# Performance work log

Hardware: AMD Instinct MI355X
Metric: run time of the kernel (lower is better)

The kernel has to match this reference:

```python
import jax, jax.numpy as jnp
import numpy as np

H, C = 4, 32          # GAT heads, per-head dim
NH = 4                # transformer heads


def layer_norm(x, g, b, eps=1e-5):
    mu = x.mean(-1, keepdims=True)
    var = ((x - mu) ** 2).mean(-1, keepdims=True)
    return (x - mu) / jnp.sqrt(var + eps) * g + b


def setup_inputs() -> dict:
    key = jax.random.key(0)
    ks = jax.random.split(key, 16)
    B, T, N, F = 256, 72, 5, 10
    D, FF = 128, 256
    # full directed graph on 5 stations, no self loops (E=20)
    ei = np.array([[i, j] for i in range(N) for j in range(N) if i != j], dtype=np.int32).T
    s = 0.1
    return {
        'x': jax.random.normal(ks[0], (B, T, N, F), jnp.float32),
        'edge_index': jnp.asarray(ei),
        'gcn_w': jax.random.normal(ks[1], (F, 64), jnp.float32) * s,
        'gcn_b': jnp.zeros((64,), jnp.float32),
        'gat_w': jax.random.normal(ks[2], (64, H * C), jnp.float32) * s,
        'gat_a_src': jax.random.normal(ks[3], (H, C), jnp.float32) * s,
        'gat_a_dst': jax.random.normal(ks[4], (H, C), jnp.float32) * s,
        'gat_b': jnp.zeros((H * C,), jnp.float32),
        'gln_g': jnp.ones((D,), jnp.float32),
        'gln_b': jnp.zeros((D,), jnp.float32),
        'tw_qkv': jax.random.normal(ks[5], (3, D, 3 * D), jnp.float32) * s,
        'tb_qkv': jnp.zeros((3, 3 * D), jnp.float32),
        'tw_o': jax.random.normal(ks[6], (3, D, D), jnp.float32) * s,
        'tb_o': jnp.zeros((3, D), jnp.float32),
        'ln1_g': jnp.ones((3, D), jnp.float32),
        'ln1_b': jnp.zeros((3, D), jnp.float32),
        'w_ff1': jax.random.normal(ks[7], (3, D, FF), jnp.float32) * s,
        'b_ff1': jnp.zeros((3, FF), jnp.float32),
        'w_ff2': jax.random.normal(ks[8], (3, FF, D), jnp.float32) * s,
        'b_ff2': jnp.zeros((3, D), jnp.float32),
        'ln2_g': jnp.ones((3, D), jnp.float32),
        'ln2_b': jnp.zeros((3, D), jnp.float32),
        'hw1': jax.random.normal(ks[9], (6, D, D // 2), jnp.float32) * s,
        'hb1': jnp.zeros((6, D // 2), jnp.float32),
        'hw2': jax.random.normal(ks[10], (6, D // 2, 5), jnp.float32) * s,
        'hb2': jnp.zeros((6, 5), jnp.float32),
    }


def reference(x, edge_index, gcn_w, gcn_b, gat_w, gat_a_src, gat_a_dst, gat_b,
              gln_g, gln_b, tw_qkv, tb_qkv, tw_o, tb_o, ln1_g, ln1_b,
              w_ff1, b_ff1, w_ff2, b_ff2, ln2_g, ln2_b, hw1, hb1, hw2, hb2):
    B, T, N, F = x.shape
    D = gln_g.shape[0]

    # ---- frozen GCN encoder (torch.no_grad): symmetric-normalized A with self loops
    src, dst = edge_index[0], edge_index[1]
    loop = jnp.arange(N, dtype=src.dtype)
    src2 = jnp.concatenate([src, loop])
    dst2 = jnp.concatenate([dst, loop])
    A = jnp.zeros((N, N), x.dtype).at[dst2, src2].add(1.0)
    deg = A.sum(1)
    dinv = jnp.where(deg > 0, deg ** -0.5, 0.0)
    Anorm = dinv[:, None] * A * dinv[None, :]
    xw = jnp.einsum('btnf,fh->btnh', x, gcn_w) + gcn_b
    gcn = jnp.tanh(jnp.einsum('ij,btjh->btih', Anorm, xw))
    gcn = jax.lax.stop_gradient(gcn)  # encoder is frozen + no_grad

    # ---- GATConv over batched graph (self loops added, PyG default), eval mode (no dropout)
    h = jnp.einsum('btnf,fhc->btnhc', gcn, gat_w.reshape(gcn.shape[-1], H, C))
    a_s = (h * gat_a_src).sum(-1)                         # [B,T,N,H]
    a_d = (h * gat_a_dst).sum(-1)
    e = a_s[:, :, src2, :] + a_d[:, :, dst2, :]           # [B,T,E2,H]
    e = jnp.where(e > 0, e, 0.2 * e)                      # LeakyReLU(0.2)
    eT = jnp.moveaxis(e, 2, 0)                            # [E2,B,T,H]
    m = jax.ops.segment_max(eT, dst2, num_segments=N)
    ex = jnp.exp(eT - m[dst2])
    denom = jax.ops.segment_sum(ex, dst2, num_segments=N)
    alpha = ex / denom[dst2]                              # scatter-softmax per dst node
    hsrc = jnp.moveaxis(h, 2, 0)[src2]                    # [E2,B,T,H,C]
    agg = jax.ops.segment_sum(alpha[..., None] * hsrc, dst2, num_segments=N)
    gat = jnp.moveaxis(agg, 0, 2).reshape(B, T, N, H * C) + gat_b
    gat = layer_norm(gat, gln_g, gln_b)

    # ---- mean-pool stations, positional encoding
    z = gat.mean(2)                                       # [B,T,D]
    pos = jnp.arange(T, dtype=jnp.float32)[:, None]
    div = jnp.exp(jnp.arange(0, D, 2, dtype=jnp.float32) * (-np.log(10000.0) / D))
    pe = jnp.zeros((T, D), x.dtype).at[:, 0::2].set(jnp.sin(pos * div)).at[:, 1::2].set(jnp.cos(pos * div))
    z = z + pe

    # ---- post-norm transformer encoder (relu FF), eval mode
    dh = D // NH
    scale = jnp.sqrt(jnp.asarray(dh, x.dtype))
    for i in range(tw_qkv.shape[0]):
        qkv = z @ tw_qkv[i] + tb_qkv[i]
        q, k, v = jnp.split(qkv, 3, axis=-1)
        q = q.reshape(B, T, NH, dh)
        k = k.reshape(B, T, NH, dh)
        v = v.reshape(B, T, NH, dh)
        att = jax.nn.softmax(jnp.einsum('bqhd,bkhd->bhqk', q, k) / scale, axis=-1)
        o = jnp.einsum('bhqk,bkhd->bqhd', att, v).reshape(B, T, D)
        z = layer_norm(z + o @ tw_o[i] + tb_o[i], ln1_g[i], ln1_b[i])
        ff = jax.nn.relu(z @ w_ff1[i] + b_ff1[i]) @ w_ff2[i] + b_ff2[i]
        z = layer_norm(z + ff, ln2_g[i], ln2_b[i])

    # ---- multi-horizon forecast heads on last timestep -> stacked [6,B,5]
    last = z[:, -1]
    h1 = jax.nn.relu(jnp.einsum('bd,kdm->kbm', last, hw1) + hb1[:, None, :])
    out = jnp.einsum('kbm,kms->kbs', h1, hw2) + hb2[:, None, :]
    return out
```

## Files before the change

### kernel.cpp

```cpp
#include <hip/hip_runtime.h>
#include <hip/hip_bf16.h>

#define B_  256
#define T_  72
#define N_  5
#define F_  10
#define D_  128
#define HH_ 4
#define CC_ 32
#define FF_ 256
#define BT_ (B_*T_)
#define E2MAX 32

#define WS_Z    256
#define WS_QKV  (WS_Z + BT_*D_)
#define WS_OBUF (WS_QKV + BT_*3*D_)
#define WS_WBF  (WS_OBUF + BT_*D_)

#define WOFF_QKV(i)  ((i)*49152)
#define WOFF_O(i)    (147456 + (i)*16384)
#define WOFF_FF1(i)  (196608 + (i)*32768)
#define WOFF_FF2(i)  (294912 + (i)*32768)
#define WOFF_GATW    393216

typedef __attribute__((ext_vector_type(8))) short bf16x8;
typedef __attribute__((ext_vector_type(4))) float f32x4;

__device__ __forceinline__ unsigned short bf16_rne(float x) {
    unsigned u = __float_as_uint(x);
    unsigned r = (u + 0x7FFFu + ((u >> 16) & 1u)) >> 16;
    return (unsigned short)r;
}
__device__ __forceinline__ unsigned bf16pk(float a, float b) {
    return (unsigned)bf16_rne(a) | ((unsigned)bf16_rne(b) << 16);
}
__device__ __forceinline__ float bf2f(short s) {
    return __uint_as_float(((unsigned)(unsigned short)s) << 16);
}

__global__ void setup_kernel(const int* __restrict__ ei, float* __restrict__ ws, int E) {
    if (threadIdx.x != 0 || blockIdx.x != 0) return;
    int* wsi = (int*)ws;
    const int N = N_;
    int E2 = E + N;
    int src2[E2MAX], dst2[E2MAX];
    for (int e = 0; e < E; ++e) { src2[e] = ei[e]; dst2[e] = ei[E + e]; }
    for (int n = 0; n < N; ++n) { src2[E + n] = n; dst2[E + n] = n; }
    float A[N_ * N_];
    for (int i = 0; i < N * N; ++i) A[i] = 0.f;
    for (int e = 0; e < E2; ++e) A[dst2[e] * N + src2[e]] += 1.f;
    float dinv[N_];
    for (int n = 0; n < N; ++n) {
        float s = 0.f;
        for (int j = 0; j < N; ++j) s += A[n * N + j];
        dinv[n] = (s > 0.f) ? rsqrtf(s) : 0.f;
    }
    for (int n = 0; n < N; ++n)
        for (int j = 0; j < N; ++j)
            ws[n * N + j] = dinv[n] * A[n * N + j] * dinv[j];
    int cnt[N_];
    for (int n = 0; n < N; ++n) cnt[n] = 0;
    for (int e = 0; e < E2; ++e) cnt[dst2[e]]++;
    int off = 0;
    for (int n = 0; n < N; ++n) { wsi[96 + n] = off; off += cnt[n]; }
    wsi[96 + N] = off;
    int cur[N_];
    for (int n = 0; n < N; ++n) cur[n] = wsi[96 + n];
    for (int e = 0; e < E2; ++e) wsi[104 + cur[dst2[e]]++] = e;
    for (int e = 0; e < E2; ++e) { wsi[32 + e] = src2[e]; wsi[64 + e] = dst2[e]; }
}
// ... 3 lines not shown
    const float* __restrict__ w_ff1, const float* __restrict__ w_ff2,
    const float* __restrict__ gat_w, short* __restrict__ wbf)
{
    __shared__ float s_t[64][65];
    const int tid = threadIdx.x;
    int t = blockIdx.x;
    const float* src; short* dst; int R, C, tr, tc;
    if (t >= 96) { int q = t - 96; src = gat_w; dst = wbf + WOFF_GATW; R = 64; C = 128; tr = 0; tc = q; }
    else {
        int layer = t / 32, r32 = t % 32;
        if (r32 < 12)      { src = tw_qkv + layer * (128*384); dst = wbf + WOFF_QKV(layer); R = 128; C = 384; tr = r32 / 6;  tc = r32 % 6; }
        else if (r32 < 16) { int q = r32 - 12; src = tw_o + layer * 16384; dst = wbf + WOFF_O(layer);  R = 128; C = 128; tr = q >> 1; tc = q & 1; }
        else if (r32 < 24) { int q = r32 - 16; src = w_ff1 + layer * 32768; dst = wbf + WOFF_FF1(layer); R = 128; C = 256; tr = q >> 2; tc = q & 3; }
        else               { int q = r32 - 24; src = w_ff2 + layer * 32768; dst = wbf + WOFF_FF2(layer); R = 256; C = 128; tr = q >> 1; tc = q & 1; }
    }
    #pragma unroll
    for (int it = 0; it < 16; ++it) {
        int e = it * 256 + tid;
        int r = e >> 6, c = e & 63;
        s_t[r][c] = src[(size_t)(tr*64 + r) * C + tc*64 + c];
    }
    __syncthreads();
    #pragma unroll
    for (int it = 0; it < 16; ++it) {
        int e = it * 256 + tid;
        int c = e >> 6, r = e & 63;
        dst[(size_t)(tc*64 + c) * R + tr*64 + r] = (short)bf16_rne(s_t[r][c]);
    }
}

__device__ __forceinline__ bf16x8 ld_frag(const short* s, int row, int kbase, int ldk) {
    return *(const bf16x8*)&s[row * ldk + (kbase ^ ((row & 7) << 3))];
}
__device__ __forceinline__ void stage_a(short* s_a, const float* __restrict__ src, int tid) {
    const float2* s2 = (const float2*)src;
    #pragma unroll
    for (int it = 0; it < 16; ++it) {
        int i2 = it * 256 + tid;
        int row = i2 >> 6, ke = (i2 & 63) * 2;
        float2 v = s2[i2];
        *(unsigned*)&s_a[row * 128 + (ke ^ ((row & 7) << 3))] = bf16pk(v.x, v.y);
    }
}
__device__ __forceinline__ void stage_b(short* s_b, const short* __restrict__ src, int tid) {
    const uint4* s4 = (const uint4*)src;
    #pragma unroll
    for (int it = 0; it < 8; ++it) {
        int c = it * 256 + tid;
        int row = c >> 4, ke = (c & 15) * 8;
        *(uint4*)&s_b[row * 128 + (ke ^ ((row & 7) << 3))] = s4[c];
    }
}

__global__ __launch_bounds__(256) void gcn_h_mfma(
    const float* __restrict__ x, const float* __restrict__ gcn_w, const float* __restrict__ gcn_b,
    const float* __restrict__ a_src, const float* __restrict__ a_dst,
    const float* __restrict__ ws, const short* __restrict__ gwT,
    short* __restrict__ hbuf, float* __restrict__ asb, float* __restrict__ adb)
{
    __shared__ float s_x[16 * 50];
    __shared__ float s_an[25];
    __shared__ short s_gcn[80 * 64];

    const int tid = threadIdx.x;
    const int tok0 = blockIdx.x * 16;

    for (int i = tid; i < 16 * 50; i += 256) s_x[i] = x[(size_t)tok0 * 50 + i];
    if (tid < 25) s_an[tid] = ws[tid];
    __syncthreads();

    #pragma unroll
    for (int it = 0; it < 2; ++it) {
        int idx = it * 256 + tid;
        int tl = idx >> 5, kp = idx & 31;
        int k0 = kp * 2;
        float w0[F_], w1[F_];
// ... 137 lines not shown
            a0 += s_alpha[wv][e][h0] * bf2f(s_h[rb + lane]);
            a1 += s_alpha[wv][e][h1] * bf2f(s_h[rb + lane + 64]);
        }
        v0[n] = a0 + gb0; v1[n] = a1 + gb1;
    }
    float r1[N_], r2[N_];
    #pragma unroll
    for (int n = 0; n < N_; ++n) { r1[n] = v0[n] + v1[n]; r2[n] = v0[n]*v0[n] + v1[n]*v1[n]; }
    #pragma unroll
    for (int mm = 1; mm < 64; mm <<= 1)
        #pragma unroll
        for (int n = 0; n < N_; ++n) { r1[n] += __shfl_xor(r1[n], mm); r2[n] += __shfl_xor(r2[n], mm); }
    float z0 = 0.f, z1 = 0.f;
    #pragma unroll
    for (int n = 0; n < N_; ++n) {
        float mu = r1[n] * (1.f / D_);
        float var = r2[n] * (1.f / D_) - mu * mu;
        float rstd = rsqrtf(var + 1e-5f);
        z0 += (v0[n] - mu) * rstd * gg0 + gB0;
        z1 += (v1[n] - mu) * rstd * gg1 + gB1;
    }
    z0 *= (1.f / N_); z1 *= (1.f / N_);
    const float cpe = -9.210340371976184f / (float)D_;
    int t = tok % T_;
    float dv0 = __expf((float)(lane & ~1) * cpe);
    float dv1 = __expf((float)((lane + 64) & ~1) * cpe);
    float ang0 = (float)t * dv0, ang1 = (float)t * dv1;
    z0 += (lane & 1) ? __cosf(ang0) : __sinf(ang0);
    z1 += (lane & 1) ? __cosf(ang1) : __sinf(ang1);
    z[(size_t)tok * D_ + lane] = z0;
    z[(size_t)tok * D_ + 64 + lane] = z1;
}

__global__ __launch_bounds__(256) void qkv_mfma(
    const float* __restrict__ z, const short* __restrict__ WT, const float* __restrict__ bias,
    float* __restrict__ qkv)
{
    __shared__ short s_a[64 * 128];
    __shared__ short s_b[128 * 128];
    const int tid = threadIdx.x;
    const int w = tid >> 6, lane = tid & 63;
    const int tok0 = blockIdx.x * 64;
    stage_a(s_a, z + (size_t)tok0 * 128, tid);
    __syncthreads();
    bf16x8 af[4];
    const int arow = w * 16 + (lane & 15);
    const int kf = (lane >> 4) * 8;
    #pragma unroll
    for (int k0 = 0; k0 < 4; ++k0) af[k0] = ld_frag(s_a, arow, k0 * 32 + kf, 128);

    for (int ch = 0; ch < 3; ++ch) {
        __syncthreads();
        stage_b(s_b, WT + ch * 128 * 128, tid);
        __syncthreads();
        #pragma unroll
        for (int n0 = 0; n0 < 8; ++n0) {
            const int ncol = ch * 128 + n0 * 16 + (lane & 15);
            const int brow = n0 * 16 + (lane & 15);
            float bv = bias[ncol];
            f32x4 acc = {bv, bv, bv, bv};
            #pragma unroll
            for (int k0 = 0; k0 < 4; ++k0) {
                bf16x8 bfg = ld_frag(s_b, brow, k0 * 32 + kf, 128);
                acc = __builtin_amdgcn_mfma_f32_16x16x32_bf16(af[k0], bfg, acc, 0, 0, 0);
            }
            const int r0 = tok0 + w * 16 + (lane >> 4) * 4;
            #pragma unroll
            for (int i = 0; i < 4; ++i)
                qkv[(size_t)(r0 + i) * 384 + ncol] = acc[i];
        }
    }
}

__global__ __launch_bounds__(256) void attn_mfma(
    const float* __restrict__ qkv, float* __restrict__ obuf)
{
    __shared__ short s_q[80 * 40];
    __shared__ short s_k[80 * 40];
    __shared__ short s_vt[32 * 104];
    __shared__ short s_p[80 * 104];

    const int bh = blockIdx.x;
    const int b = bh >> 2, h = bh & 3;
    const int tid = threadIdx.x;
    const int w = tid >> 6, lane = tid & 63;
    const int c = lane & 15, g = lane >> 4;
    const float* base = qkv + (size_t)b * T_ * 384 + h * 32;

    for (int idx = tid; idx < 80 * 32; idx += 256) {
        int row = idx >> 5, cc = idx & 31;
        float qv = 0.f, kv = 0.f;
        if (row < T_) {
            qv = base[row * 384 + cc];
            kv = base[row * 384 + 128 + cc];
        }
        s_q[row * 40 + cc] = (short)bf16_rne(qv);
        s_k[row * 40 + cc] = (short)bf16_rne(kv);
    }
    for (int idx = tid; idx < 80 * 32; idx += 256) {
        int key = idx >> 5, cc = idx & 31;
        float vv = (key < T_) ? base[key * 384 + 256 + cc] : 0.f;
        s_vt[cc * 104 + key] = (short)bf16_rne(vv);
    }
    for (int idx = tid; idx < 32 * 24; idx += 256) {
        int cc = idx / 24, key = 80 + idx % 24;
        s_vt[cc * 104 + key] = 0;
    }
    for (int idx = tid; idx < 80 * 24; idx += 256) {
        int row = idx / 24, col = 80 + idx % 24;
        s_p[row * 104 + col] = 0;
    }
    __syncthreads();

    const float scale = 0.17677669529663687f;

    for (int m = w; m < 5; m += 4) {
        bf16x8 aq = *(const bf16x8*)&s_q[(m * 16 + c) * 40 + g * 8];
        f32x4 accS[5];
        #pragma unroll
        for (int n0 = 0; n0 < 5; ++n0) {
            bf16x8 bk = *(const bf16x8*)&s_k[(n0 * 16 + c) * 40 + g * 8];
            f32x4 z4 = {0,0,0,0};
            accS[n0] = __builtin_amdgcn_mfma_f32_16x16x32_bf16(aq, bk, z4, 0, 0, 0);
        }
        float ps[5][4];
        float mx[4], den[4];
        #pragma unroll
        for (int i = 0; i < 4; ++i) mx[i] = -1e30f;
        #pragma unroll
        for (int n0 = 0; n0 < 5; ++n0)
            #pragma unroll
            for (int i = 0; i < 4; ++i) {
                float s = accS[n0][i] * scale;
                if (n0 == 4 && c >= 8) s = -1e30f;
                ps[n0][i] = s;
                mx[i] = fmaxf(mx[i], s);
            }
        #pragma unroll
        for (int mm = 1; mm < 16; mm <<= 1)
            #pragma unroll
            for (int i = 0; i < 4; ++i) mx[i] = fmaxf(mx[i], __shfl_xor(mx[i], mm));
        #pragma unroll
        for (int i = 0; i < 4; ++i) den[i] = 0.f;
        #pragma unroll
        for (int n0 = 0; n0 < 5; ++n0)
            #pragma unroll
            for (int i = 0; i < 4; ++i) {
                float e = __expf(ps[n0][i] - mx[i]);
                ps[n0][i] = e;
                den[i] += e;
            }
        #pragma unroll
        for (int mm = 1; mm < 16; mm <<= 1)
            #pragma unroll
            for (int i = 0; i < 4; ++i) den[i] += __shfl_xor(den[i], mm);
        float rden[4];
        #pragma unroll
        for (int i = 0; i < 4; ++i) rden[i] = 1.f / den[i];
        #pragma unroll
        for (int n0 = 0; n0 < 5; ++n0)
            #pragma unroll
            for (int i = 0; i < 4; ++i) {
                int row = m * 16 + g * 4 + i;
                s_p[row * 104 + n0 * 16 + c] = (short)bf16_rne(ps[n0][i] * rden[i]);
            }
        f32x4 accO[2] = {{0,0,0,0},{0,0,0,0}};
        #pragma unroll
        for (int kt = 0; kt < 3; ++kt) {
            bf16x8 ap = *(const bf16x8*)&s_p[(m * 16 + c) * 104 + kt * 32 + g * 8];
            #pragma unroll
            for (int n0 = 0; n0 < 2; ++n0) {
                bf16x8 bv = *(const bf16x8*)&s_vt[(n0 * 16 + c) * 104 + kt * 32 + g * 8];
                accO[n0] = __builtin_amdgcn_mfma_f32_16x16x32_bf16(ap, bv, accO[n0], 0, 0, 0);
            }
        }
        #pragma unroll
        for (int n0 = 0; n0 < 2; ++n0)
            #pragma unroll
            for (int i = 0; i < 4; ++i) {
                int row = m * 16 + g * 4 + i;
                if (row < T_)
                    obuf[(size_t)(b * T_ + row) * D_ + h * 32 + n0 * 16 + c] = accO[n0][i];
            }
    }
}

__global__ __launch_bounds__(256) void oproj_ff_mfma(
    const float* __restrict__ obuf, const short* __restrict__ WoT, const float* __restrict__ bo,
    const float* __restrict__ g1, const float* __restrict__ be1,
    const short* __restrict__ W1T, const float* __restrict__ b1,
    const short* __restrict__ W2T, const float* __restrict__ b2,
    const float* __restrict__ g2, const float* __restrict__ be2,
    float* __restrict__ z)
{
    __shared__ short s_a[64 * 128];
    __shared__ short s_b[128 * 128];
    __shared__ short s_f[64 * 256];
    const int tid = threadIdx.x;
    const int w = tid >> 6, lane = tid & 63;
    const int tok0 = blockIdx.x * 64;
    const int cbase = lane & 15;
    const int arow = w * 16 + cbase;
    const int kf = (lane >> 4) * 8;
    const int r0 = tok0 + w * 16 + (lane >> 4) * 4;
    const int lrow0 = w * 16 + (lane >> 4) * 4;

    stage_a(s_a, obuf + (size_t)tok0 * 128, tid);
    stage_b(s_b, WoT, tid);
    __syncthreads();
    bf16x8 af[4];
    #pragma unroll
    for (int k0 = 0; k0 < 4; ++k0) af[k0] = ld_frag(s_a, arow, k0 * 32 + kf, 128);

    f32x4 acc[8];
    #pragma unroll
    for (int n0 = 0; n0 < 8; ++n0) {
        float bv = bo[n0 * 16 + cbase];
        acc[n0] = (f32x4){bv, bv, bv, bv};
        const int brow = n0 * 16 + cbase;
        #pragma unroll
        for (int k0 = 0; k0 < 4; ++k0) {
            bf16x8 bfg = ld_frag(s_b, brow, k0 * 32 + kf, 128);
            acc[n0] = __builtin_amdgcn_mfma_f32_16x16x32_bf16(af[k0], bfg, acc[n0], 0, 0, 0);
        }
    }
    #pragma unroll
    for (int n0 = 0; n0 < 8; ++n0)
        #pragma unroll
        for (int i = 0; i < 4; ++i)
            acc[n0][i] += z[(size_t)(r0 + i) * 128 + n0 * 16 + cbase];
    {
        float s1[4] = {0,0,0,0}, s2[4] = {0,0,0,0};
        #pragma unroll
        for (int n0 = 0; n0 < 8; ++n0)
            #pragma unroll
            for (int i = 0; i < 4; ++i) { float v = acc[n0][i]; s1[i] += v; s2[i] += v * v; }
        #pragma unroll
        for (int m = 1; m < 16; m <<= 1)
            #pragma unroll
            for (int i = 0; i < 4; ++i) { s1[i] += __shfl_xor(s1[i], m); s2[i] += __shfl_xor(s2[i], m); }
        #pragma unroll
        for (int i = 0; i < 4; ++i) {
            float mu = s1[i] * (1.f / D_);
            float var = s2[i] * (1.f / D_) - mu * mu;
            float rstd = rsqrtf(var + 1e-5f);
            #pragma unroll
            for (int n0 = 0; n0 < 8; ++n0) {
                float gv = g1[n0 * 16 + cbase], bev = be1[n0 * 16 + cbase];
                acc[n0][i] = (acc[n0][i] - mu) * rstd * gv + bev;
            }
        }
    }
    #pragma unroll
    for (int n0 = 0; n0 < 8; ++n0)
        #pragma unroll
        for (int i = 0; i < 4; ++i) {
            int row = lrow0 + i;
            s_a[row * 128 + ((n0 * 16 + cbase) ^ ((row & 7) << 3))] = (short)bf16_rne(acc[n0][i]);
        }
    bf16x8 af1[4];
    #pragma unroll
    for (int k0 = 0; k0 < 4; ++k0) af1[k0] = ld_frag(s_a, arow, k0 * 32 + kf, 128);

    for (int ch = 0; ch < 2; ++ch) {
        __syncthreads();
        stage_b(s_b, W1T + ch * 128 * 128, tid);
        __syncthreads();
        #pragma unroll
        for (int n0 = 0; n0 < 8; ++n0) {
            const int ncol = ch * 128 + n0 * 16 + cbase;
            const int brow = n0 * 16 + cbase;
            float bv = b1[ncol];
            f32x4 a = {bv, bv, bv, bv};
            #pragma unroll
            for (int k0 = 0; k0 < 4; ++k0) {
                bf16x8 bfg = ld_frag(s_b, brow, k0 * 32 + kf, 128);
                a = __builtin_amdgcn_mfma_f32_16x16x32_bf16(af1[k0], bfg, a, 0, 0, 0);
            }
            #pragma unroll
            for (int i = 0; i < 4; ++i) {
                int row = lrow0 + i;
                s_f[row * 256 + (ncol ^ ((row & 7) << 3))] = (short)bf16_rne(fmaxf(a[i], 0.f));
            }
        }
    }
    f32x4 acc2[8];
    #pragma unroll
    for (int n0 = 0; n0 < 8; ++n0) {
        float bv = b2[n0 * 16 + cbase];
        acc2[n0] = (f32x4){bv, bv, bv, bv};
    }
    for (int kc = 0; kc < 2; ++kc) {
        __syncthreads();
        #pragma unroll
        for (int it = 0; it < 8; ++it) {
            int cc = it * 256 + tid;
            int row = cc >> 4, ke = (cc & 15) * 8;
            uint4 v = *(const uint4*)&W2T[row * 256 + kc * 128 + ke];
            *(uint4*)&s_b[row * 128 + (ke ^ ((row & 7) << 3))] = v;
        }
        __syncthreads();
        bf16x8 af2[4];
        #pragma unroll
        for (int k0 = 0; k0 < 4; ++k0)
            af2[k0] = ld_frag(s_f, arow, kc * 128 + k0 * 32 + kf, 256);
        #pragma unroll
        for (int n0 = 0; n0 < 8; ++n0) {
            const int brow = n0 * 16 + cbase;
            #pragma unroll
            for (int k0 = 0; k0 < 4; ++k0) {
                bf16x8 bfg = ld_frag(s_b, brow, k0 * 32 + kf, 128);
                acc2[n0] = __builtin_amdgcn_mfma_f32_16x16x32_bf16(af2[k0], bfg, acc2[n0], 0, 0, 0);
            }
        }
    }
    #pragma unroll
    for (int n0 = 0; n0 < 8; ++n0)
        #pragma unroll
        for (int i = 0; i < 4; ++i)
            acc2[n0][i] += acc[n0][i];
    float s1[4] = {0,0,0,0}, s2[4] = {0,0,0,0};
    #pragma unroll
    for (int n0 = 0; n0 < 8; ++n0)
        #pragma unroll
        for (int i = 0; i < 4; ++i) { float v = acc2[n0][i]; s1[i] += v; s2[i] += v * v; }
    #pragma unroll
    for (int m = 1; m < 16; m <<= 1)
        #pragma unroll
        for (int i = 0; i < 4; ++i) { s1[i] += __shfl_xor(s1[i], m); s2[i] += __shfl_xor(s2[i], m); }
    #pragma unroll
    for (int i = 0; i < 4; ++i) {
        float mu = s1[i] * (1.f / D_);
        float var = s2[i] * (1.f / D_) - mu * mu;
        float rstd = rsqrtf(var + 1e-5f);
        #pragma unroll
        for (int n0 = 0; n0 < 8; ++n0) {
            float gv = g2[n0 * 16 + cbase], bev = be2[n0 * 16 + cbase];
            z[(size_t)(r0 + i) * 128 + n0 * 16 + cbase] = (acc2[n0][i] - mu) * rstd * gv + bev;
        }
    }
}

__global__ __launch_bounds__(64) void heads_kernel(
    const float* __restrict__ z, const float* __restrict__ hw1, const float* __restrict__ hb1,
    const float* __restrict__ hw2, const float* __restrict__ hb2, float* __restrict__ out)
{
    const int k = blockIdx.x >> 8;
    const int b = blockIdx.x & 255;
    const int tid = threadIdx.x;
    __shared__ float s_last[D_];
    __shared__ float s_h1[64];
    const float* zr = z + (size_t)(b * T_ + (T_ - 1)) * D_;
    s_last[tid] = zr[tid];
    s_last[tid + 64] = zr[tid + 64];
    __syncthreads();
    float acc = hb1[k * 64 + tid];
    const float* w1 = hw1 + (size_t)k * D_ * 64;
    for (int dd = 0; dd < D_; ++dd) acc += s_last[dd] * w1[dd * 64 + tid];
    s_h1[tid] = fmaxf(acc, 0.f);
    __syncthreads();
    if (tid < 5) {
        float o = hb2[k * 5 + tid];
        const float* w2 = hw2 + (size_t)k * 64 * 5;
        for (int j = 0; j < 64; ++j) o += s_h1[j] * w2[j * 5 + tid];
        out[(size_t)k * (B_ * 5) + b * 5 + tid] = o;
    }
}

extern "C" void kernel_launch(void* const* d_in, const int* in_sizes, int n_in,
                              void* d_out, int out_size, void* d_ws, size_t ws_size,
                              hipStream_t stream) {
    const float* x      = (const float*)d_in[0];
    const int*   ei     = (const int*)  d_in[1];
    const float* gcn_w  = (const float*)d_in[2];
    const float* gcn_b  = (const float*)d_in[3];
    const float* gat_w  = (const float*)d_in[4];
    const float* a_src  = (const float*)d_in[5];
    const float* a_dst  = (const float*)d_in[6];
    const float* gat_b  = (const float*)d_in[7];
    const float* gln_g  = (const float*)d_in[8];
    const float* gln_b  = (const float*)d_in[9];
    const float* tw_qkv = (const float*)d_in[10];
    const float* tb_qkv = (const float*)d_in[11];
    const float* tw_o   = (const float*)d_in[12];
    const float* tb_o   = (const float*)d_in[13];
    const float* ln1_g  = (const float*)d_in[14];
    const float* ln1_b  = (const float*)d_in[15];
    const float* w_ff1  = (const float*)d_in[16];
    const float* b_ff1  = (const float*)d_in[17];
    const float* w_ff2  = (const float*)d_in[18];
    const float* b_ff2  = (const float*)d_in[19];
    const float* ln2_g  = (const float*)d_in[20];
    const float* ln2_b  = (const float*)d_in[21];
    const float* hw1    = (const float*)d_in[22];
    const float* hb1    = (const float*)d_in[23];
    const float* hw2    = (const float*)d_in[24];
    const float* hb2    = (const float*)d_in[25];
    float* out = (float*)d_out;
    float* ws  = (float*)d_ws;

    float* z    = ws + WS_Z;
    float* qkv  = ws + WS_QKV;
    float* obuf = ws + WS_OBUF;
    short* wbf  = (short*)(ws + WS_WBF);

    short* hbuf = (short*)(ws + WS_QKV);
    float* asb  = ws + WS_OBUF;
    float* adb  = ws + WS_OBUF + BT_ * 5 * 4;

    const int E = in_sizes[1] / 2;
    const int E2 = E + N_;

    setup_kernel<<<1, 64, 0, stream>>>(ei, ws, E);
    prep_kernel<<<98, 256, 0, stream>>>(tw_qkv, tw_o, w_ff1, w_ff2, gat_w, wbf);
    gcn_h_mfma<<<BT_ / 16, 256, 0, stream>>>(x, gcn_w, gcn_b, a_src, a_dst, ws,
                                             wbf + WOFF_GATW, hbuf, asb, adb);
    gat_agg<<<BT_ / 4, 256, 0, stream>>>(hbuf, asb, adb, gat_b, gln_g, gln_b, ws, z, E2);
    for (int i = 0; i < 3; ++i) {
        qkv_mfma<<<BT_ / 64, 256, 0, stream>>>(z, wbf + WOFF_QKV(i),
                                               tb_qkv + (size_t)i * 3 * D_, qkv);
        attn_mfma<<<B_ * HH_, 256, 0, stream>>>(qkv, obuf);
        oproj_ff_mfma<<<BT_ / 64, 256, 0, stream>>>(obuf, wbf + WOFF_O(i),
                                                    tb_o + (size_t)i * D_,
                                                    ln1_g + (size_t)i * D_, ln1_b + (size_t)i * D_,
                                                    wbf + WOFF_FF1(i), b_ff1 + (size_t)i * FF_,
                                                    wbf + WOFF_FF2(i), b_ff2 + (size_t)i * D_,
                                                    ln2_g + (size_t)i * D_, ln2_b + (size_t)i * D_, z);
    }
    heads_kernel<<<6 * B_, 64, 0, stream>>>(z, hw1, hb1, hw2, hb2, out);
}
```

Baseline: 342.6 us.

## Fuse all transformer layers and forecast heads into one per-sequence kernel

Replaces the per-layer qkv, attention and oproj/FF kernels and the heads kernel with a single kernel. Each block owns one sequence of 72 tokens and keeps activations, Q/K/V, attention output and FF intermediates in about 160KB of LDS across all three layers. This removes global round-trips of qkv/obuf/z between kernels and about ten launches. The cost is one block per CU with 256 threads and only 256 blocks, so occupancy is low. Every block also restages weights from global/L2, and the 72-row tile is padded to 80.

```diff
diff --git a/kernel.cpp b/kernel.cpp
--- a/kernel.cpp
+++ b/kernel.cpp
@@ -23,6 +23,14 @@
 #define WOFF_FF2(i)  (294912 + (i)*32768)
 #define WOFF_GATW    393216
 
+#define MZF_OFF   0
+#define MSB_OFF   38016
+#define MSQ_OFF   70784
+#define MSK_OFF   92544
+#define MVT_OFF   114304
+#define MOB_OFF   140928
+#define MSMEM_BYTES 162688
+
 typedef __attribute__((ext_vector_type(8))) short bf16x8;
 typedef __attribute__((ext_vector_type(4))) float f32x4;
 
@@ -36,6 +44,12 @@
 }
 __device__ __forceinline__ float bf2f(short s) {
     return __uint_as_float(((unsigned)(unsigned short)s) << 16);
+}
+__device__ __forceinline__ bf16x8 cvt8(const float* p) {
+    float4 a = *(const float4*)p;
+    float4 b = *(const float4*)(p + 4);
+    unsigned u[4] = {bf16pk(a.x, a.y), bf16pk(a.z, a.w), bf16pk(b.x, b.y), bf16pk(b.z, b.w)};
+    return *(bf16x8*)u;
 }
 
 __global__ void setup_kernel(const int* __restrict__ ei, float* __restrict__ ws, int E) {
@@ -105,16 +119,6 @@
 __device__ __forceinline__ bf16x8 ld_frag(const short* s, int row, int kbase, int ldk) {
     return *(const bf16x8*)&s[row * ldk + (kbase ^ ((row & 7) << 3))];
 }
-__device__ __forceinline__ void stage_a(short* s_a, const float* __restrict__ src, int tid) {
-    const float2* s2 = (const float2*)src;
-    #pragma unroll
-    for (int it = 0; it < 16; ++it) {
-        int i2 = it * 256 + tid;
-        int row = i2 >> 6, ke = (i2 & 63) * 2;
-        float2 v = s2[i2];
-        *(unsigned*)&s_a[row * 128 + (ke ^ ((row & 7) << 3))] = bf16pk(v.x, v.y);
-    }
-}
 __device__ __forceinline__ void stage_b(short* s_b, const short* __restrict__ src, int tid) {
     const uint4* s4 = (const uint4*)src;
     #pragma unroll
@@ -318,338 +322,378 @@
     z[(size_t)tok * D_ + 64 + lane] = z1;
 }
 
-__global__ __launch_bounds__(256) void qkv_mfma(
-    const float* __restrict__ z, const short* __restrict__ WT, const float* __restrict__ bias,
-    float* __restrict__ qkv)
+__global__ __launch_bounds__(256, 1) void layers_fused(
+    const float* __restrict__ zg, const short* __restrict__ wbf,
+    const float* __restrict__ tb_qkv, const float* __restrict__ tb_o,
+    const float* __restrict__ ln1_g, const float* __restrict__ ln1_b,
+    const float* __restrict__ b_ff1, const float* __restrict__ b_ff2,
+    const float* __restrict__ ln2_g, const float* __restrict__ ln2_b,
+    const float* __restrict__ hw1, const float* __restrict__ hb1,
+    const float* __restrict__ hw2, const float* __restrict__ hb2,
+    float* __restrict__ out)
 {
-    __shared__ short s_a[64 * 128];
-    __shared__ short s_b[128 * 128];
-    const int tid = threadIdx.x;
-    const int w = tid >> 6, lane = tid & 63;
-    const int tok0 = blockIdx.x * 64;
-    stage_a(s_a, z + (size_t)tok0 * 128, tid);
-    __syncthreads();
-    bf16x8 af[4];
-    const int arow = w * 16 + (lane & 15);
-    const int kf = (lane >> 4) * 8;
-    #pragma unroll
-    for (int k0 = 0; k0 < 4; ++k0) af[k0] = ld_frag(s_a, arow, k0 * 32 + kf, 128);
-
-    for (int ch = 0; ch < 3; ++ch) {
-        __syncthreads();
-        stage_b(s_b, WT + ch * 128 * 128, tid);
-        __syncthreads();
-        #pragma unroll
-        for (int n0 = 0; n0 < 8; ++n0) {
-            const int ncol = ch * 128 + n0 * 16 + (lane & 15);
-            const int brow = n0 * 16 + (lane & 15);
-            float bv = bias[ncol];
-            f32x4 acc = {bv, bv, bv, bv};
-            #pragma unroll
-            for (int k0 = 0; k0 < 4; ++k0) {
-                bf16x8 bfg = ld_frag(s_b, brow, k0 * 32 + kf, 128);
-                acc = __builtin_amdgcn_mfma_f32_16x16x32_bf16(af[k0], bfg, acc, 0, 0, 0);
-            }
-            const int r0 = tok0 + w * 16 + (lane >> 4) * 4;
-            #pragma unroll
-            for (int i = 0; i < 4; ++i)
-                qkv[(size_t)(r0 + i) * 384 + ncol] = acc[i];
-        }
-    }
-}
-
-__global__ __launch_bounds__(256) void attn_mfma(
-    const float* __restrict__ qkv, float* __restrict__ obuf)
-{
-    __shared__ short s_q[80 * 40];
-    __shared__ short s_k[80 * 40];
-    __shared__ short s_vt[32 * 104];
-    __shared__ short s_p[80 * 104];
-
-    const int bh = blockIdx.x;
-    const int b = bh >> 2, h = bh & 3;
+    extern __shared__ char smem[];
+    float* s_zf = (float*)(smem + MZF_OFF);
+    short* s_b  = (short*)(smem + MSB_OFF);
+    short* s_q  = (short*)(smem + MSQ_OFF);
+    short* s_k  = (short*)(smem + MSK_OFF);
+    short* s_vt = (short*)(smem + MVT_OFF);
+    short* s_ob = (short*)(smem + MOB_OFF);
+    short* s_f  = s_q;
+    short* s_z1 = s_vt;
+
     const int tid = threadIdx.x;
     const int w = tid >> 6, lane = tid & 63;
     const int c = lane & 15, g = lane >> 4;
-    const float* base = qkv + (size_t)b * T_ * 384 + h * 32;
-
-    for (int idx = tid; idx < 80 * 32; idx += 256) {
-        int row = idx >> 5, cc = idx & 31;
-        float qv = 0.f, kv = 0.f;
-        if (row < T_) {
-            qv = base[row * 384 + cc];
-            kv = base[row * 384 + 128 + cc];
-        }
-        s_q[row * 40 + cc] = (short)bf16_rne(qv);
-        s_k[row * 40 + cc] = (short)bf16_rne(kv);
-    }
-    for (int idx = tid; idx < 80 * 32; idx += 256) {
-        int key = idx >> 5, cc = idx & 31;
-        float vv = (key < T_) ? base[key * 384 + 256 + cc] : 0.f;
-        s_vt[cc * 104 + key] = (short)bf16_rne(vv);
-    }
-    for (int idx = tid; idx < 32 * 24; idx += 256) {
-        int cc = idx / 24, key = 80 + idx % 24;
-        s_vt[cc * 104 + key] = 0;
-    }
-    for (int idx = tid; idx < 80 * 24; idx += 256) {
-        int row = idx / 24, col = 80 + idx % 24;
-        s_p[row * 104 + col] = 0;
+    const int kf = g * 8;
+    const int b = blockIdx.x;
+
+    for (int idx = tid; idx < 72 * 128; idx += 256) {
+        int r = idx >> 7, col = idx & 127;
+        s_zf[r * 132 + col] = zg[(size_t)(b * T_ + r) * D_ + col];
+    }
+    for (int idx = tid; idx < 128 * 32; idx += 256) {
+        int ch = idx >> 5, key = 72 + (idx & 31);
+        s_vt[ch * 104 + key] = 0;
     }
     __syncthreads();
 
-    const float scale = 0.17677669529663687f;
-
-    for (int m = w; m < 5; m += 4) {
-        bf16x8 aq = *(const bf16x8*)&s_q[(m * 16 + c) * 40 + g * 8];
-        f32x4 accS[5];
-        #pragma unroll
-        for (int n0 = 0; n0 < 5; ++n0) {
-            bf16x8 bk = *(const bf16x8*)&s_k[(n0 * 16 + c) * 40 + g * 8];
-            f32x4 z4 = {0,0,0,0};
-            accS[n0] = __builtin_amdgcn_mfma_f32_16x16x32_bf16(aq, bk, z4, 0, 0, 0);
-        }
-        float ps[5][4];
-        float mx[4], den[4];
-        #pragma unroll
-        for (int i = 0; i < 4; ++i) mx[i] = -1e30f;
-        #pragma unroll
-        for (int n0 = 0; n0 < 5; ++n0)
+    for (int L = 0; L < 3; ++L) {
+        const short* Wq = wbf + WOFF_QKV(L);
+        const short* Wo = wbf + WOFF_O(L);
+        const short* W1 = wbf + WOFF_FF1(L);
+        const short* W2 = wbf + WOFF_FF2(L);
+        const float* bq = tb_qkv + L * 384;
+        const float* bo = tb_o + L * D_;
+        const float* g1 = ln1_g + L * D_, *be1 = ln1_b + L * D_;
+        const float* b1 = b_ff1 + L * FF_, *b2 = b_ff2 + L * D_;
+        const float* g2 = ln2_g + L * D_, *be2 = ln2_b + L * D_;
+
+        for (int ch = 0; ch < 3; ++ch) {
+            __syncthreads();
+            stage_b(s_b, Wq + ch * 16384, tid);
+            __syncthreads();
+            bf16x8 Bf[2][4];
+            float bvj[2];
+            #pragma unroll
+            for (int j = 0; j < 2; ++j) {
+                int n0 = w * 2 + j;
+                int brow = n0 * 16 + c;
+                #pragma unroll
+                for (int k0 = 0; k0 < 4; ++k0) Bf[j][k0] = ld_frag(s_b, brow, k0 * 32 + kf, 128);
+                bvj[j] = bq[ch * 128 + n0 * 16 + c];
+            }
+            #pragma unroll
+            for (int m = 0; m < 5; ++m) {
+                int arow = m * 16 + c;
+                bool valid = arow < 72;
+                bf16x8 Af[4];
+                bf16x8 z8 = {0,0,0,0,0,0,0,0};
+                #pragma unroll
+                for (int k0 = 0; k0 < 4; ++k0)
+                    Af[k0] = valid ? cvt8(&s_zf[arow * 132 + k0 * 32 + kf]) : z8;
+                #pragma unroll
+                for (int j = 0; j < 2; ++j) {
+                    int n0 = w * 2 + j;
+                    f32x4 acc = {bvj[j], bvj[j], bvj[j], bvj[j]};
+                    #pragma unroll
+                    for (int k0 = 0; k0 < 4; ++k0)
+                        acc = __builtin_amdgcn_mfma_f32_16x16x32_bf16(Af[k0], Bf[j][k0], acc, 0, 0, 0);
+                    int wcol = n0 * 16 + c;
+                    #pragma unroll
+                    for (int i = 0; i < 4; ++i) {
+                        int lrow = m * 16 + g * 4 + i;
+                        short v = (short)bf16_rne(acc[i]);
+                        if (ch == 0)      s_q[lrow * 136 + wcol] = v;
+                        else if (ch == 1) s_k[lrow * 136 + wcol] = v;
+                        else              s_vt[wcol * 104 + lrow] = v;
+                    }
+                }
+            }
+        }
+        __syncthreads();
+
+        {
+            short* pstrip = s_b + w * 16 * 104;
+            for (int t2 = lane; t2 < 16 * 16; t2 += 64) {
+                int r = t2 >> 4, col = 80 + (t2 & 15);
+                pstrip[r * 104 + col] = 0;
+            }
+            const float scale = 0.17677669529663687f;
+            #pragma unroll
+            for (int m = 0; m < 5; ++m) {
+                bf16x8 aq = *(const bf16x8*)&s_q[(m * 16 + c) * 136 + w * 32 + kf];
+                float ps[5][4], mx[4], den[4];
+                #pragma unroll
+                for (int i = 0; i < 4; ++i) mx[i] = -1e30f;
+                #pragma unroll
+                for (int n0 = 0; n0 < 5; ++n0) {
+                    bf16x8 bk = *(const bf16x8*)&s_k[(n0 * 16 + c) * 136 + w * 32 + kf];
+                    f32x4 z4 = {0,0,0,0};
+                    f32x4 accS = __builtin_amdgcn_mfma_f32_16x16x32_bf16(aq, bk, z4, 0, 0, 0);
+                    #pragma unroll
+                    for (int i = 0; i < 4; ++i) {
+                        float s = accS[i] * scale;
+                        if (n0 == 4 && c >= 8) s = -1e30f;
+                        ps[n0][i] = s;
+                        mx[i] = fmaxf(mx[i], s);
+                    }
+                }
+                #pragma unroll
+                for (int mm = 1; mm < 16; mm <<= 1)
+                    #pragma unroll
+                    for (int i = 0; i < 4; ++i) mx[i] = fmaxf(mx[i], __shfl_xor(mx[i], mm));
+                #pragma unroll
+                for (int i = 0; i < 4; ++i) den[i] = 0.f;
+                #pragma unroll
+                for (int n0 = 0; n0 < 5; ++n0)
+                    #pragma unroll
+                    for (int i = 0; i < 4; ++i) { float e = __expf(ps[n0][i] - mx[i]); ps[n0][i] = e; den[i] += e; }
+                #pragma unroll
+                for (int mm = 1; mm < 16; mm <<= 1)
+                    #pragma unroll
+                    for (int i = 0; i < 4; ++i) den[i] += __shfl_xor(den[i], mm);
+                float rden[4];
+                #pragma unroll
+                for (int i = 0; i < 4; ++i) rden[i] = 1.f / den[i];
+                #pragma unroll
+                for (int n0 = 0; n0 < 5; ++n0)
+                    #pragma unroll
+                    for (int i = 0; i < 4; ++i)
+                        pstrip[(g * 4 + i) * 104 + n0 * 16 + c] = (short)bf16_rne(ps[n0][i] * rden[i]);
+                f32x4 accO[2] = {{0,0,0,0},{0,0,0,0}};
+                #pragma unroll
+                for (int kt = 0; kt < 3; ++kt) {
+                    bf16x8 ap = *(const bf16x8*)&pstrip[c * 104 + kt * 32 + kf];
+                    #pragma unroll
+                    for (int n0 = 0; n0 < 2; ++n0) {
+                        bf16x8 bv = *(const bf16x8*)&s_vt[(w * 32 + n0 * 16 + c) * 104 + kt * 32 + kf];
+                        accO[n0] = __builtin_amdgcn_mfma_f32_16x16x32_bf16(ap, bv, accO[n0], 0, 0, 0);
+                    }
+                }
+                #pragma unroll
+                for (int n0 = 0; n0 < 2; ++n0)
+                    #pragma unroll
+                    for (int i = 0; i < 4; ++i)
+                        s_ob[(m * 16 + g * 4 + i) * 136 + w * 32 + n0 * 16 + c] = (short)bf16_rne(accO[n0][i]);
+            }
+        }
+        __syncthreads();
+
+        stage_b(s_b, Wo, tid);
+        __syncthreads();
+        for (int m = w; m < 5; m += 4) {
+            bf16x8 Af[4];
+            #pragma unroll
+            for (int k0 = 0; k0 < 4; ++k0)
+                Af[k0] = *(const bf16x8*)&s_ob[(m * 16 + c) * 136 + k0 * 32 + kf];
+            f32x4 acc[8];
+            #pragma unroll
+            for (int n0 = 0; n0 < 8; ++n0) {
+                float bv = bo[n0 * 16 + c];
+                acc[n0] = (f32x4){bv, bv, bv, bv};
+                int brow = n0 * 16 + c;
+                #pragma unroll
+                for (int k0 = 0; k0 < 4; ++k0) {
+                    bf16x8 bfg = ld_frag(s_b, brow, k0 * 32 + kf, 128);
+                    acc[n0] = __builtin_amdgcn_mfma_f32_16x16x32_bf16(Af[k0], bfg, acc[n0], 0, 0, 0);
+                }
+            }
+            #pragma unroll
+            for (int n0 = 0; n0 < 8; ++n0)
+                #pragma unroll
+                for (int i = 0; i < 4; ++i) {
+                    int row = m * 16 + g * 4 + i;
+                    acc[n0][i] += (row < 72) ? s_zf[row * 132 + n0 * 16 + c] : 0.f;
+                }
+            float s1[4] = {0,0,0,0}, s2[4] = {0,0,0,0};
+            #pragma unroll
+            for (int n0 = 0; n0 < 8; ++n0)
+                #pragma unroll
+                for (int i = 0; i < 4; ++i) { float v = acc[n0][i]; s1[i] += v; s2[i] += v * v; }
+            #pragma unroll
+            for (int mm = 1; mm < 16; mm <<= 1)
+                #pragma unroll
+                for (int i = 0; i < 4; ++i) { s1[i] += __shfl_xor(s1[i], mm); s2[i] += __shfl_xor(s2[i], mm); }
             #pragma unroll
             for (int i = 0; i < 4; ++i) {
-                float s = accS[n0][i] * scale;
-                if (n0 == 4 && c >= 8) s = -1e30f;
-                ps[n0][i] = s;
-                mx[i] = fmaxf(mx[i], s);
-            }
-        #pragma unroll
-        for (int mm = 1; mm < 16; mm <<= 1)
-            #pragma unroll
-            for (int i = 0; i < 4; ++i) mx[i] = fmaxf(mx[i], __shfl_xor(mx[i], mm));
-        #pragma unroll
-        for (int i = 0; i < 4; ++i) den[i] = 0.f;
-        #pragma unroll
-        for (int n0 = 0; n0 < 5; ++n0)
+                float mu = s1[i] * (1.f / D_);
+                float var = s2[i] * (1.f / D_) - mu * mu;
+                float rstd = rsqrtf(var + 1e-5f);
+                int row = m * 16 + g * 4 + i;
+                #pragma unroll
+                for (int n0 = 0; n0 < 8; ++n0) {
+                    float v = (acc[n0][i] - mu) * rstd * g1[n0 * 16 + c] + be1[n0 * 16 + c];
+                    if (row < 72) s_zf[row * 132 + n0 * 16 + c] = v;
+                    s_z1[row * 136 + n0 * 16 + c] = (short)bf16_rne(v);
+                }
+            }
+        }
+
+        for (int ch = 0; ch < 2; ++ch) {
+            __syncthreads();
+            stage_b(s_b, W1 + ch * 16384, tid);
+            __syncthreads();
+            bf16x8 Bf[2][4];
+            float bvj[2];
+            #pragma unroll
+            for (int j = 0; j < 2; ++j) {
+                int n0 = w * 2 + j;
+                int brow = n0 * 16 + c;
+                #pragma unroll
+                for (int k0 = 0; k0 < 4; ++k0) Bf[j][k0] = ld_frag(s_b, brow, k0 * 32 + kf, 128);
+                bvj[j] = b1[ch * 128 + n0 * 16 + c];
+            }
+            #pragma unroll
+            for (int m = 0; m < 5; ++m) {
+                bf16x8 Af[4];
+                #pragma unroll
+                for (int k0 = 0; k0 < 4; ++k0)
+                    Af[k0] = *(const bf16x8*)&s_z1[(m * 16 + c) * 136 + k0 * 32 + kf];
+                #pragma unroll
+                for (int j = 0; j < 2; ++j) {
+                    int n0 = w * 2 + j;
+                    f32x4 acc = {bvj[j], bvj[j], bvj[j], bvj[j]};
+                    #pragma unroll
+                    for (int k0 = 0; k0 < 4; ++k0)
+                        acc = __builtin_amdgcn_mfma_f32_16x16x32_bf16(Af[k0], Bf[j][k0], acc, 0, 0, 0);
+                    #pragma unroll
+                    for (int i = 0; i < 4; ++i) {
+                        int lrow = m * 16 + g * 4 + i;
+                        s_f[lrow * 264 + ch * 128 + n0 * 16 + c] = (short)bf16_rne(fmaxf(acc[i], 0.f));
+                    }
+                }
+            }
+        }
+
+        f32x4 accA[8], accB[8];
+        #pragma unroll
+        for (int n0 = 0; n0 < 8; ++n0) {
+            float bv = b2[n0 * 16 + c];
+            accA[n0] = (f32x4){bv, bv, bv, bv};
+            accB[n0] = (f32x4){bv, bv, bv, bv};
+        }
+        for (int kc = 0; kc < 2; ++kc) {
+            __syncthreads();
+            {
+                #pragma unroll
+                for (int it = 0; it < 8; ++it) {
+                    int cc = it * 256 + tid;
+                    int row = cc >> 4, ke = (cc & 15) * 8;
+                    uint4 v = *(const uint4*)&W2[row * 256 + kc * 128 + ke];
+                    *(uint4*)&s_b[row * 128 + (ke ^ ((row & 7) << 3))] = v;
+                }
+            }
+            __syncthreads();
+            {
+                bf16x8 Af[4];
+                #pragma unroll
+                for (int k0 = 0; k0 < 4; ++k0)
+                    Af[k0] = *(const bf16x8*)&s_f[(w * 16 + c) * 264 + kc * 128 + k0 * 32 + kf];
+                #pragma unroll
+                for (int n0 = 0; n0 < 8; ++n0) {
+                    int brow = n0 * 16 + c;
+                    #pragma unroll
+                    for (int k0 = 0; k0 < 4; ++k0) {
+                        bf16x8 bfg = ld_frag(s_b, brow, k0 * 32 + kf, 128);
+                        accA[n0] = __builtin_amdgcn_mfma_f32_16x16x32_bf16(Af[k0], bfg, accA[n0], 0, 0, 0);
+                    }
+                }
+            }
+            if (w == 0) {
+                bf16x8 Af[4];
+                #pragma unroll
+                for (int k0 = 0; k0 < 4; ++k0)
+                    Af[k0] = *(const bf16x8*)&s_f[(64 + c) * 264 + kc * 128 + k0 * 32 + kf];
+                #pragma unroll
+                for (int n0 = 0; n0 < 8; ++n0) {
+                    int brow = n0 * 16 + c;
+                    #pragma unroll
+                    for (int k0 = 0; k0 < 4; ++k0) {
+                        bf16x8 bfg = ld_frag(s_b, brow, k0 * 32 + kf, 128);
+                        accB[n0] = __builtin_amdgcn_mfma_f32_16x16x32_bf16(Af[k0], bfg, accB[n0], 0, 0, 0);
+                    }
+                }
+            }
+        }
+        {
+            #pragma unroll
+            for (int n0 = 0; n0 < 8; ++n0)
+                #pragma unroll
+                for (int i = 0; i < 4; ++i) {
+                    int row = w * 16 + g * 4 + i;
+                    accA[n0][i] += (row < 72) ? s_zf[row * 132 + n0 * 16 + c] : 0.f;
+                }
+            float s1[4] = {0,0,0,0}, s2[4] = {0,0,0,0};
+            #pragma unroll
+            for (int n0 = 0; n0 < 8; ++n0)
+                #pragma unroll
+                for (int i = 0; i < 4; ++i) { float v = accA[n0][i]; s1[i] += v; s2[i] += v * v; }
+            #pragma unroll
+            for (int mm = 1; mm < 16; mm <<= 1)
+                #pragma unroll
+                for (int i = 0; i < 4; ++i) { s1[i] += __shfl_xor(s1[i], mm); s2[i] += __shfl_xor(s2[i], mm); }
             #pragma unroll
             for (int i = 0; i < 4; ++i) {
-                float e = __expf(ps[n0][i] - mx[i]);
-                ps[n0][i] = e;
-                den[i] += e;
-            }
-        #pragma unroll
-        for (int mm = 1; mm < 16; mm <<= 1)
-            #pragma unroll
-            for (int i = 0; i < 4; ++i) den[i] += __shfl_xor(den[i], mm);
-        float rden[4];
-        #pragma unroll
-        for (int i = 0; i < 4; ++i) rden[i] = 1.f / den[i];
-        #pragma unroll
-        for (int n0 = 0; n0 < 5; ++n0)
+                float mu = s1[i] * (1.f / D_);
+                float var = s2[i] * (1.f / D_) - mu * mu;
+                float rstd = rsqrtf(var + 1e-5f);
+                int row = w * 16 + g * 4 + i;
+                if (row < 72)
+                    #pragma unroll
+                    for (int n0 = 0; n0 < 8; ++n0)
+                        s_zf[row * 132 + n0 * 16 + c] =
+                            (accA[n0][i] - mu) * rstd * g2[n0 * 16 + c] + be2[n0 * 16 + c];
+            }
+        }
+        if (w == 0) {
+            #pragma unroll
+            for (int n0 = 0; n0 < 8; ++n0)
+                #pragma unroll
+                for (int i = 0; i < 4; ++i) {
+                    int row = 64 + g * 4 + i;
+                    accB[n0][i] += (row < 72) ? s_zf[row * 132 + n0 * 16 + c] : 0.f;
+                }
+            float s1[4] = {0,0,0,0}, s2[4] = {0,0,0,0};
+            #pragma unroll
+            for (int n0 = 0; n0 < 8; ++n0)
+                #pragma unroll
+                for (int i = 0; i < 4; ++i) { float v = accB[n0][i]; s1[i] += v; s2[i] += v * v; }
+            #pragma unroll
+            for (int mm = 1; mm < 16; mm <<= 1)
+                #pragma unroll
+                for (int i = 0; i < 4; ++i) { s1[i] += __shfl_xor(s1[i], mm); s2[i] += __shfl_xor(s2[i], mm); }
             #pragma unroll
             for (int i = 0; i < 4; ++i) {
-                int row = m * 16 + g * 4 + i;
-                s_p[row * 104 + n0 * 16 + c] = (short)bf16_rne(ps[n0][i] * rden[i]);
-            }
-        f32x4 accO[2] = {{0,0,0,0},{0,0,0,0}};
-        #pragma unroll
-        for (int kt = 0; kt < 3; ++kt) {
-            bf16x8 ap = *(const bf16x8*)&s_p[(m * 16 + c) * 104 + kt * 32 + g * 8];
-            #pragma unroll
-            for (int n0 = 0; n0 < 2; ++n0) {
-                bf16x8 bv = *(const bf16x8*)&s_vt[(n0 * 16 + c) * 104 + kt * 32 + g * 8];
-                accO[n0] = __builtin_amdgcn_mfma_f32_16x16x32_bf16(ap, bv, accO[n0], 0, 0, 0);
-            }
-        }
-        #pragma unroll
-        for (int n0 = 0; n0 < 2; ++n0)
-            #pragma unroll
-            for (int i = 0; i < 4; ++i) {
-                int row = m * 16 + g * 4 + i;
-                if (row < T_)
-                    obuf[(size_t)(b * T_ + row) * D_ + h * 32 + n0 * 16 + c] = accO[n0][i];
-            }
-    }
-}
-
-__global__ __launch_bounds__(256) void oproj_ff_mfma(
-    const float* __restrict__ obuf, const short* __restrict__ WoT, const float* __restrict__ bo,
-    const float* __restrict__ g1, const float* __restrict__ be1,
-    const short* __restrict__ W1T, const float* __restrict__ b1,
-    const short* __restrict__ W2T, const float* __restrict__ b2,
-    const float* __restrict__ g2, const float* __restrict__ be2,
-    float* __restrict__ z)
-{
-    __shared__ short s_a[64 * 128];
-    __shared__ short s_b[128 * 128];
-    __shared__ short s_f[64 * 256];
-    const int tid = threadIdx.x;
-    const int w = tid >> 6, lane = tid & 63;
-    const int tok0 = blockIdx.x * 64;
-    const int cbase = lane & 15;
-    const int arow = w * 16 + cbase;
-    const int kf = (lane >> 4) * 8;
-    const int r0 = tok0 + w * 16 + (lane >> 4) * 4;
-    const int lrow0 = w * 16 + (lane >> 4) * 4;
-
-    stage_a(s_a, obuf + (size_t)tok0 * 128, tid);
-    stage_b(s_b, WoT, tid);
+                float mu = s1[i] * (1.f / D_);
+                float var = s2[i] * (1.f / D_) - mu * mu;
+                float rstd = rsqrtf(var + 1e-5f);
+                int row = 64 + g * 4 + i;
+                if (row < 72)
+                    #pragma unroll
+                    for (int n0 = 0; n0 < 8; ++n0)
+                        s_zf[row * 132 + n0 * 16 + c] =
+                            (accB[n0][i] - mu) * rstd * g2[n0 * 16 + c] + be2[n0 * 16 + c];
+            }
+        }
+    }
+
     __syncthreads();
-    bf16x8 af[4];
-    #pragma unroll
-    for (int k0 = 0; k0 < 4; ++k0) af[k0] = ld_frag(s_a, arow, k0 * 32 + kf, 128);
-
-    f32x4 acc[8];
-    #pragma unroll
-    for (int n0 = 0; n0 < 8; ++n0) {
-        float bv = bo[n0 * 16 + cbase];
-        acc[n0] = (f32x4){bv, bv, bv, bv};
-        const int brow = n0 * 16 + cbase;
-        #pragma unroll
-        for (int k0 = 0; k0 < 4; ++k0) {
-            bf16x8 bfg = ld_frag(s_b, brow, k0 * 32 + kf, 128);
-            acc[n0] = __builtin_amdgcn_mfma_f32_16x16x32_bf16(af[k0], bfg, acc[n0], 0, 0, 0);
-        }
-    }
-    #pragma unroll
-    for (int n0 = 0; n0 < 8; ++n0)
-        #pragma unroll
-        for (int i = 0; i < 4; ++i)
-            acc[n0][i] += z[(size_t)(r0 + i) * 128 + n0 * 16 + cbase];
-    {
-        float s1[4] = {0,0,0,0}, s2[4] = {0,0,0,0};
-        #pragma unroll
-        for (int n0 = 0; n0 < 8; ++n0)
-            #pragma unroll
-            for (int i = 0; i < 4; ++i) { float v = acc[n0][i]; s1[i] += v; s2[i] += v * v; }
-        #pragma unroll
-        for (int m = 1; m < 16; m <<= 1)
-            #pragma unroll
-            for (int i = 0; i < 4; ++i) { s1[i] += __shfl_xor(s1[i], m); s2[i] += __shfl_xor(s2[i], m); }
-        #pragma unroll
-        for (int i = 0; i < 4; ++i) {
-            float mu = s1[i] * (1.f / D_);
-            float var = s2[i] * (1.f / D_) - mu * mu;
-            float rstd = rsqrtf(var + 1e-5f);
-            #pragma unroll
-            for (int n0 = 0; n0 < 8; ++n0) {
-                float gv = g1[n0 * 16 + cbase], bev = be1[n0 * 16 + cbase];
-                acc[n0][i] = (acc[n0][i] - mu) * rstd * gv + bev;
-            }
-        }
-    }
-    #pragma unroll
-    for (int n0 = 0; n0 < 8; ++n0)
-        #pragma unroll
-        for (int i = 0; i < 4; ++i) {
-            int row = lrow0 + i;
-            s_a[row * 128 + ((n0 * 16 + cbase) ^ ((row & 7) << 3))] = (short)bf16_rne(acc[n0][i]);
-        }
-    bf16x8 af1[4];
-    #pragma unroll
-    for (int k0 = 0; k0 < 4; ++k0) af1[k0] = ld_frag(s_a, arow, k0 * 32 + kf, 128);
-
-    for (int ch = 0; ch < 2; ++ch) {
-        __syncthreads();
-        stage_b(s_b, W1T + ch * 128 * 128, tid);
-        __syncthreads();
-        #pragma unroll
-        for (int n0 = 0; n0 < 8; ++n0) {
-            const int ncol = ch * 128 + n0 * 16 + cbase;
-            const int brow = n0 * 16 + cbase;
-            float bv = b1[ncol];
-            f32x4 a = {bv, bv, bv, bv};
-            #pragma unroll
-            for (int k0 = 0; k0 < 4; ++k0) {
-                bf16x8 bfg = ld_frag(s_b, brow, k0 * 32 + kf, 128);
-                a = __builtin_amdgcn_mfma_f32_16x16x32_bf16(af1[k0], bfg, a, 0, 0, 0);
-            }
-            #pragma unroll
-            for (int i = 0; i < 4; ++i) {
-                int row = lrow0 + i;
-                s_f[row * 256 + (ncol ^ ((row & 7) << 3))] = (short)bf16_rne(fmaxf(a[i], 0.f));
-            }
-        }
-    }
-    f32x4 acc2[8];
-    #pragma unroll
-    for (int n0 = 0; n0 < 8; ++n0) {
-        float bv = b2[n0 * 16 + cbase];
-        acc2[n0] = (f32x4){bv, bv, bv, bv};
-    }
-    for (int kc = 0; kc < 2; ++kc) {
-        __syncthreads();
-        #pragma unroll
-        for (int it = 0; it < 8; ++it) {
-            int cc = it * 256 + tid;
-            int row = cc >> 4, ke = (cc & 15) * 8;
-            uint4 v = *(const uint4*)&W2T[row * 256 + kc * 128 + ke];
-            *(uint4*)&s_b[row * 128 + (ke ^ ((row & 7) << 3))] = v;
-        }
-        __syncthreads();
-        bf16x8 af2[4];
-        #pragma unroll
-        for (int k0 = 0; k0 < 4; ++k0)
-            af2[k0] = ld_frag(s_f, arow, kc * 128 + k0 * 32 + kf, 256);
-        #pragma unroll
-        for (int n0 = 0; n0 < 8; ++n0) {
-            const int brow = n0 * 16 + cbase;
-            #pragma unroll
-            for (int k0 = 0; k0 < 4; ++k0) {
-                bf16x8 bfg = ld_frag(s_b, brow, k0 * 32 + kf, 128);
-                acc2[n0] = __builtin_amdgcn_mfma_f32_16x16x32_bf16(af2[k0], bfg, acc2[n0], 0, 0, 0);
-            }
-        }
-    }
-    #pragma unroll
-    for (int n0 = 0; n0 < 8; ++n0)
-        #pragma unroll
-        for (int i = 0; i < 4; ++i)
-            acc2[n0][i] += acc[n0][i];
-    float s1[4] = {0,0,0,0}, s2[4] = {0,0,0,0};
-    #pragma unroll
-    for (int n0 = 0; n0 < 8; ++n0)
-        #pragma unroll
-        for (int i = 0; i < 4; ++i) { float v = acc2[n0][i]; s1[i] += v; s2[i] += v * v; }
-    #pragma unroll
-    for (int m = 1; m < 16; m <<= 1)
-        #pragma unroll
-        for (int i = 0; i < 4; ++i) { s1[i] += __shfl_xor(s1[i], m); s2[i] += __shfl_xor(s2[i], m); }
-    #pragma unroll
-    for (int i = 0; i < 4; ++i) {
-        float mu = s1[i] * (1.f / D_);
-        float var = s2[i] * (1.f / D_) - mu * mu;
-        float rstd = rsqrtf(var + 1e-5f);
-        #pragma unroll
-        for (int n0 = 0; n0 < 8; ++n0) {
-            float gv = g2[n0 * 16 + cbase], bev = be2[n0 * 16 + cbase];
-            z[(size_t)(r0 + i) * 128 + n0 * 16 + cbase] = (acc2[n0][i] - mu) * rstd * gv + bev;
-        }
-    }
-}
-
-__global__ __launch_bounds__(64) void heads_kernel(
-    const float* __restrict__ z, const float* __restrict__ hw1, const float* __restrict__ hb1,
-    const float* __restrict__ hw2, const float* __restrict__ hb2, float* __restrict__ out)
-{
-    const int k = blockIdx.x >> 8;
-    const int b = blockIdx.x & 255;
-    const int tid = threadIdx.x;
-    __shared__ float s_last[D_];
-    __shared__ float s_h1[64];
-    const float* zr = z + (size_t)(b * T_ + (T_ - 1)) * D_;
-    s_last[tid] = zr[tid];
-    s_last[tid + 64] = zr[tid + 64];
+    float* s_h1 = (float*)s_b;
+    for (int t2 = tid; t2 < 384; t2 += 256) {
+        int k = t2 >> 6, j = t2 & 63;
+        float acc = hb1[k * 64 + j];
+        const float* w1p = hw1 + (size_t)k * D_ * 64 + j;
+        for (int d = 0; d < D_; ++d) acc += s_zf[71 * 132 + d] * w1p[d * 64];
+        s_h1[k * 64 + j] = fmaxf(acc, 0.f);
+    }
     __syncthreads();
-    float acc = hb1[k * 64 + tid];
-    const float* w1 = hw1 + (size_t)k * D_ * 64;
-    for (int dd = 0; dd < D_; ++dd) acc += s_last[dd] * w1[dd * 64 + tid];
-    s_h1[tid] = fmaxf(acc, 0.f);
-    __syncthreads();
-    if (tid < 5) {
-        float o = hb2[k * 5 + tid];
-        const float* w2 = hw2 + (size_t)k * 64 * 5;
-        for (int j = 0; j < 64; ++j) o += s_h1[j] * w2[j * 5 + tid];
-        out[(size_t)k * (B_ * 5) + b * 5 + tid] = o;
+    if (tid < 30) {
+        int k = tid / 5, s = tid % 5;
+        float o = hb2[k * 5 + s];
+        const float* w2p = hw2 + (size_t)k * 64 * 5 + s;
+        for (int j = 0; j < 64; ++j) o += s_h1[k * 64 + j] * w2p[j * 5];
+        out[(size_t)k * (B_ * 5) + b * 5 + s] = o;
     }
 }
 
@@ -685,10 +729,8 @@
     float* out = (float*)d_out;
     float* ws  = (float*)d_ws;
 
-    float* z    = ws + WS_Z;
-    float* qkv  = ws + WS_QKV;
-    float* obuf = ws + WS_OBUF;
-    short* wbf  = (short*)(ws + WS_WBF);
+    float* z   = ws + WS_Z;
+    short* wbf = (short*)(ws + WS_WBF);
 
     short* hbuf = (short*)(ws + WS_QKV);
     float* asb  = ws + WS_OBUF;
@@ -696,22 +738,20 @@
 
     const int E = in_sizes[1] / 2;
     const int E2 = E + N_;
+
+    static bool attr_set = false;
+    if (!attr_set) {
+        hipFuncSetAttribute((const void*)layers_fused,
+                            hipFuncAttributeMaxDynamicSharedMemorySize, MSMEM_BYTES);
+        attr_set = true;
+    }
 
     setup_kernel<<<1, 64, 0, stream>>>(ei, ws, E);
     prep_kernel<<<98, 256, 0, stream>>>(tw_qkv, tw_o, w_ff1, w_ff2, gat_w, wbf);
     gcn_h_mfma<<<BT_ / 16, 256, 0, stream>>>(x, gcn_w, gcn_b, a_src, a_dst, ws,
                                              wbf + WOFF_GATW, hbuf, asb, adb);
     gat_agg<<<BT_ / 4, 256, 0, stream>>>(hbuf, asb, adb, gat_b, gln_g, gln_b, ws, z, E2);
-    for (int i = 0; i < 3; ++i) {
-        qkv_mfma<<<BT_ / 64, 256, 0, stream>>>(z, wbf + WOFF_QKV(i),
-                                               tb_qkv + (size_t)i * 3 * D_, qkv);
-        attn_mfma<<<B_ * HH_, 256, 0, stream>>>(qkv, obuf);
-        oproj_ff_mfma<<<BT_ / 64, 256, 0, stream>>>(obuf, wbf + WOFF_O(i),
-                                                    tb_o + (size_t)i * D_,
-                                                    ln1_g + (size_t)i * D_, ln1_b + (size_t)i * D_,
-                                                    wbf + WOFF_FF1(i), b_ff1 + (size_t)i * FF_,
-                                                    wbf + WOFF_FF2(i), b_ff2 + (size_t)i * D_,
-                                                    ln2_g + (size_t)i * D_, ln2_b + (size_t)i * D_, z);
-    }
-    heads_kernel<<<6 * B_, 64, 0, stream>>>(z, hw1, hb1, hw2, hb2, out);
-}
+    layers_fused<<<B_, 256, MSMEM_BYTES, stream>>>(z, wbf, tb_qkv, tb_o,
+                                                   ln1_g, ln1_b, b_ff1, b_ff2,
+                                                   ln2_g, ln2_b, hw1, hb1, hw2, hb2, out);
+}
```

After: 355.6 us. +3.8%, slower.
